# Optimization experiments

Hardware: AMD Instinct MI355X
Metric: run time of the kernel (lower is better)

## Reference

```python
import jax, jax.numpy as jnp
import numpy as np

D = 768      # embedding_dim
H = 12       # num_heads
HS = D // H  # head_size = 64
B, T, TC = 8, 1024, 256
FF = 4 * D
EPS = 1e-5


def _layernorm(x, w, b):
    mu = jnp.mean(x, axis=-1, keepdims=True)
    var = jnp.mean((x - mu) ** 2, axis=-1, keepdims=True)
    return (x - mu) / jnp.sqrt(var + EPS) * w + b


def _mha(x_q, x_kv, Wq, bq, Wk, bk, Wv, bv):
    # Batched equivalent of the per-head Python loop: weights stacked as [H, D, HS].
    q = jnp.einsum('btd,hde->bhte', x_q, Wq) + bq[None, :, None, :]
    k = jnp.einsum('bsd,hde->bhse', x_kv, Wk) + bk[None, :, None, :]
    v = jnp.einsum('bsd,hde->bhse', x_kv, Wv) + bv[None, :, None, :]
    scale = HS ** (-0.5)  # original scales by C**-0.5 with C = head_size
    wei = jax.nn.softmax(jnp.einsum('bhte,bhse->bhts', q, k) * scale, axis=-1)
    o = jnp.einsum('bhts,bhse->bhte', wei, v)  # [B,H,T,HS]
    # torch.cat over heads on dim=-1 == transpose then merge head dims
    return o.transpose(0, 2, 1, 3).reshape(o.shape[0], o.shape[2], H * HS)


def setup_inputs() -> dict:
    key = jax.random.key(0)
    ks = jax.random.split(key, 20)
    s = 0.02
    inp = {
        'img_embedding': jax.random.normal(ks[0], (B, T, D), jnp.float32),
        'context': jax.random.normal(ks[1], (B, TC, D), jnp.float32),
        'ln1_w': jnp.ones((D,), jnp.float32), 'ln1_b': jnp.zeros((D,), jnp.float32),
        'sWq': jax.random.normal(ks[2], (H, D, HS), jnp.float32) * s,
        'sbq': jnp.zeros((H, HS), jnp.float32),
        'sWk': jax.random.normal(ks[3], (H, D, HS), jnp.float32) * s,
        'sbk': jnp.zeros((H, HS), jnp.float32),
        'sWv': jax.random.normal(ks[4], (H, D, HS), jnp.float32) * s,
        'sbv': jnp.zeros((H, HS), jnp.float32),
        'ln2_w': jnp.ones((D,), jnp.float32), 'ln2_b': jnp.zeros((D,), jnp.float32),
        'cWq': jax.random.normal(ks[5], (H, D, HS), jnp.float32) * s,
        'cbq': jnp.zeros((H, HS), jnp.float32),
        'cWk': jax.random.normal(ks[6], (H, D, HS), jnp.float32) * s,
        'cbk': jnp.zeros((H, HS), jnp.float32),
        'cWv': jax.random.normal(ks[7], (H, D, HS), jnp.float32) * s,
        'cbv': jnp.zeros((H, HS), jnp.float32),
        'ln3_w': jnp.ones((D,), jnp.float32), 'ln3_b': jnp.zeros((D,), jnp.float32),
        'W1': jax.random.normal(ks[8], (D, FF), jnp.float32) * s,
        'b1': jnp.zeros((FF,), jnp.float32),
        'W2': jax.random.normal(ks[9], (FF, D), jnp.float32) * s,
        'b2': jnp.zeros((D,), jnp.float32),
    }
    return inp


def reference(img_embedding, context, ln1_w, ln1_b, sWq, sbq, sWk, sbk, sWv, sbv,
              ln2_w, ln2_b, cWq, cbq, cWk, cbk, cWv, cbv, ln3_w, ln3_b,
              W1, b1, W2, b2):
    x = img_embedding
    x = x + _mha(_layernorm(x, ln1_w, ln1_b), _layernorm(x, ln1_w, ln1_b),
                 sWq, sbq, sWk, sbk, sWv, sbv)
    x = x + _mha(_layernorm(x, ln2_w, ln2_b), context,
                 cWq, cbq, cWk, cbk, cWv, cbv)
    h = _layernorm(x, ln3_w, ln3_b)
    ff = jax.nn.silu(h @ W1 + b1) @ W2 + b2
    return x + ff
```

## Files before the change

kernel.cpp:

```cpp
#include <hip/hip_runtime.h>
#include <hip/hip_bf16.h>


#define D_EMB 768
#define N_HEADS 12
#define HEAD 64
#define B_SZ 8
#define T_IMG 1024
#define T_CTX 256
#define FF_DIM 3072
#define ROWS_IMG (B_SZ * T_IMG)
#define ROWS_CTX (B_SZ * T_CTX)
#define BIGCOL (1 << 28)
#define PART_STRIDE (ROWS_IMG * D_EMB)

typedef __bf16 bf16x8 __attribute__((ext_vector_type(8)));
typedef __bf16 bf16x4 __attribute__((ext_vector_type(4)));
typedef float f32x4 __attribute__((ext_vector_type(4)));

__device__ __forceinline__ void gld16(const void* g, void* l) {
    __builtin_amdgcn_global_load_lds(
        (const __attribute__((address_space(1))) unsigned int*)g,
        (__attribute__((address_space(3))) unsigned int*)l, 16, 0, 0);
}

__global__ __launch_bounds__(256) void reduce_w2_kernel(
    const __bf16* __restrict__ P, const float* __restrict__ b2,
    float* __restrict__ X) {
    int i = blockIdx.x * 256 + threadIdx.x;
    int base = i * 4;
    int col = base % D_EMB;
    bf16x4 p0 = *(const bf16x4*)&P[base];
    bf16x4 p1 = *(const bf16x4*)&P[PART_STRIDE + base];
    float4 x = *(float4*)&X[base];
    float4 bb = *(const float4*)&b2[col];
    x.x += (float)p0[0] + (float)p1[0] + bb.x;
    x.y += (float)p0[1] + (float)p1[1] + bb.y;
    x.z += (float)p0[2] + (float)p1[2] + bb.z;
    x.w += (float)p0[3] + (float)p1[3] + bb.w;
    *(float4*)&X[base] = x;
}

__device__ __forceinline__ void transpose_cvt_body(
    float (*tile)[65], const float* __restrict__ src, __bf16* __restrict__ dst,
    int src_rows, int src_cols, int bx, int by, int tid) {
    int r0 = by * 64, c0 = bx * 64;
    int lr = tid >> 4, lc = (tid & 15) * 4;
#pragma unroll
    for (int i = 0; i < 4; i++) {
        float4 v = *(const float4*)&src[(size_t)(r0 + i * 16 + lr) * src_cols + c0 + lc];
        tile[i * 16 + lr][lc] = v.x; tile[i * 16 + lr][lc + 1] = v.y;
        tile[i * 16 + lr][lc + 2] = v.z; tile[i * 16 + lr][lc + 3] = v.w;
    }
    __syncthreads();
#pragma unroll
    for (int i = 0; i < 4; i++) {
        int cc = i * 16 + lr;
        int rr = (tid & 15) * 4;
        bf16x4 o;
#pragma unroll
        for (int j = 0; j < 4; j++) o[j] = (__bf16)tile[rr + j][cc];
        *(bf16x4*)&dst[(size_t)(c0 + cc) * src_rows + r0 + rr] = o;
    }
}

__device__ __forceinline__ void repack_body(
    float (*tile)[65],
    const float* __restrict__ Wq, const float* __restrict__ Wk,
    const float* __restrict__ Wv, const float* __restrict__ bq,
    const float* __restrict__ bk, const float* __restrict__ bv,
    __bf16* __restrict__ Wt, float* __restrict__ bp, int bx, int byy, int tid) {
    int which = byy / 12, h = byy - which * 12;
    int d0 = bx * 64;
    const float* W = (which == 0) ? Wq : ((which == 1) ? Wk : Wv);
    const float* src = W + ((size_t)h * D_EMB + d0) * HEAD;
    int lr = tid >> 4, lc = (tid & 15) * 4;
#pragma unroll
    for (int i = 0; i < 4; i++) {
        float4 v = *(const float4*)&src[(size_t)(i * 16 + lr) * HEAD + lc];
        tile[i * 16 + lr][lc] = v.x; tile[i * 16 + lr][lc + 1] = v.y;
        tile[i * 16 + lr][lc + 2] = v.z; tile[i * 16 + lr][lc + 3] = v.w;
    }
    __syncthreads();
#pragma unroll
    for (int i = 0; i < 4; i++) {
        int e = i * 16 + lr;
        int dd = (tid & 15) * 4;
        bf16x4 o;
#pragma unroll
        for (int j = 0; j < 4; j++) o[j] = (__bf16)tile[dd + j][e];
        *(bf16x4*)&Wt[(size_t)(which * 768 + h * 64 + e) * D_EMB + d0 + dd] = o;
    }
    if (bx == 0 && tid < 64) {
        const float* bb = (which == 0) ? bq : ((which == 1) ? bk : bv);
        bp[which * 768 + h * 64 + tid] = bb[h * 64 + tid];
    }
}

__global__ __launch_bounds__(256) void preproc_kernel(
    const float* __restrict__ ctx, __bf16* __restrict__ ctxb,
    const float* __restrict__ sWq, const float* __restrict__ sWk,
    const float* __restrict__ sWv, const float* __restrict__ sbq,
    const float* __restrict__ sbk, const float* __restrict__ sbv,
    __bf16* __restrict__ Wt, float* __restrict__ bp,
    const float* __restrict__ cWq, const float* __restrict__ cWk,
    const float* __restrict__ cWv, const float* __restrict__ cbq,
    const float* __restrict__ cbk, const float* __restrict__ cbv,
    __bf16* __restrict__ cWt, float* __restrict__ cbp,
    const float* __restrict__ W1, __bf16* __restrict__ W1t,
    const float* __restrict__ W2, __bf16* __restrict__ W2t) {
    __shared__ float tile[64][65];
    int bid = blockIdx.x;
    int tid = threadIdx.x;
    if (bid < 1536) {
        int i = bid * 256 + tid;
        float4 v = ((const float4*)ctx)[i];
        __bf16* d = ctxb + i * 4;
        d[0] = (__bf16)v.x; d[1] = (__bf16)v.y; d[2] = (__bf16)v.z; d[3] = (__bf16)v.w;
    } else if (bid < 1968) {
        int vb = bid - 1536;
        repack_body(tile, sWq, sWk, sWv, sbq, sbk, sbv, Wt, bp,
                    vb % 12, vb / 12, tid);
    } else if (bid < 2400) {
        int vb = bid - 1968;
        repack_body(tile, cWq, cWk, cWv, cbq, cbk, cbv, cWt, cbp,
                    vb % 12, vb / 12, tid);
    } else if (bid < 2976) {
        int vb = bid - 2400;
        transpose_cvt_body(tile, W1, W1t, 768, FF_DIM, vb % 48, vb / 48, tid);
    } else {
        int vb = bid - 2976;
        transpose_cvt_body(tile, W2, W2t, FF_DIM, 768, vb % 12, vb / 12, tid);
    }
}

__global__ __launch_bounds__(256) void ln_kernel(const float* __restrict__ x,
                                                 const float* __restrict__ lw,
                                                 const float* __restrict__ lb,
                                                 __bf16* __restrict__ y) {
    int row = blockIdx.x;
    int tid = threadIdx.x;
    const float* xr = x + (size_t)row * D_EMB;
    float a0 = xr[tid], a1 = xr[tid + 256], a2 = xr[tid + 512];
    float s = a0 + a1 + a2;
    float ss = a0 * a0 + a1 * a1 + a2 * a2;
#pragma unroll
    for (int off = 32; off > 0; off >>= 1) {
        s += __shfl_down(s, off, 64);
        ss += __shfl_down(ss, off, 64);
    }
    __shared__ float red[8];
    __shared__ float stats[2];
    int wv = tid >> 6, lane = tid & 63;
    if (lane == 0) { red[wv] = s; red[4 + wv] = ss; }
    __syncthreads();
    if (tid == 0) {
        float S = red[0] + red[1] + red[2] + red[3];
        float SS = red[4] + red[5] + red[6] + red[7];
        float mu = S * (1.0f / D_EMB);
        float var = SS * (1.0f / D_EMB) - mu * mu;
        stats[0] = mu;
        stats[1] = rsqrtf(var + 1e-5f);
    }
    __syncthreads();
    float mu = stats[0], rs = stats[1];
    __bf16* yr = y + (size_t)row * D_EMB;
    yr[tid]       = (__bf16)((a0 - mu) * rs * lw[tid]       + lb[tid]);
    yr[tid + 256] = (__bf16)((a1 - mu) * rs * lw[tid + 256] + lb[tid + 256]);
    yr[tid + 512] = (__bf16)((a2 - mu) * rs * lw[tid + 512] + lb[tid + 512]);
}

__device__ __forceinline__ bf16x8 lds_frag(const __bf16* h, int row, int kk, int quad) {
    int off = (kk * 32 + quad * 8) ^ ((row & 7) << 3);
    return *(const bf16x8*)&h[row * 64 + off];
}

template <int LDA, int LDB>
__device__ __forceinline__ void gemm_body(
    int bx, int by, int kz, int tid,
    const __bf16* __restrict__ A,
    const __bf16* __restrict__ Bt,
    const float* __restrict__ bias,
    __bf16* __restrict__ Cb, int ldc,
    int Kc, int act, int qlimit,
    __bf16* __restrict__ VTout, int vtok, int vcol0, int kcol0, int kcol1,
    float* __restrict__ Xres,
    __bf16* As, __bf16* Bs) {
    int w = tid >> 6, lane = tid & 63;
    int c = lane & 15, quad = lane >> 4;
    int wm = (w >> 1) * 64, wn = (w & 1) * 64;

    f32x4 acc[4][4];
#pragma unroll
    for (int i = 0; i < 4; i++)
#pragma unroll
        for (int j = 0; j < 4; j++) acc[i][j] = (f32x4){0.f, 0.f, 0.f, 0.f};

    int srow = tid >> 3;
    int scol = ((tid & 7) * 8) ^ ((srow & 7) * 8);
    const __bf16* Ag = A + (size_t)(by * 128 + srow) * LDA + (size_t)kz * Kc + scol;
    const __bf16* Bg = Bt + (size_t)(bx * 128 + srow) * LDB + (size_t)kz * Kc + scol;
    char* AsB = (char*)As + w * 1024;
    char* BsB = (char*)Bs + w * 1024;

    for (int k0 = 0; k0 < Kc; k0 += 64) {
#pragma unroll
        for (int j = 0; j < 4; j++) {
            gld16(Ag + (size_t)(j * 32) * LDA + k0, AsB + j * 4096);
            gld16(Bg + (size_t)(j * 32) * LDB + k0, BsB + j * 4096);
        }
        __syncthreads();
#pragma unroll
        for (int kk = 0; kk < 2; kk++) {
            bf16x8 af[4], bfr[4];
#pragma unroll
            for (int mi = 0; mi < 4; mi++)
                af[mi] = lds_frag(As, wm + mi * 16 + c, kk, quad);
#pragma unroll
            for (int ni = 0; ni < 4; ni++)
                bfr[ni] = lds_frag(Bs, wn + ni * 16 + c, kk, quad);
#pragma unroll
            for (int mi = 0; mi < 4; mi++)
#pragma unroll
                for (int ni = 0; ni < 4; ni++)
                    acc[mi][ni] = __builtin_amdgcn_mfma_f32_16x16x32_bf16(
                        bfr[ni], af[mi], acc[mi][ni], 0, 0, 0);
        }
        __syncthreads();
    }

#pragma unroll
    for (int mi = 0; mi < 4; mi++) {
#pragma unroll
        for (int ni = 0; ni < 4; ni++) {
            int row = by * 128 + wm + mi * 16 + c;
            int colbase = bx * 128 + wn + ni * 16 + quad * 4;
            float bvv[4] = {0.f, 0.f, 0.f, 0.f};
            if (bias && kz == 0) {
                float4 b4 = *(const float4*)&bias[colbase];
                bvv[0] = b4.x; bvv[1] = b4.y; bvv[2] = b4.z; bvv[3] = b4.w;
            }
            float qs = (colbase < qlimit) ? 0.125f : 1.0f;
            float v[4];
#pragma unroll
            for (int r = 0; r < 4; r++) {
                float t = (acc[mi][ni][r] + bvv[r]) * qs;
                if (act == 1) t = t / (1.0f + __expf(-t));
                v[r] = t;
            }
            if (Xres) {
                float4 x4 = *(float4*)&Xres[(size_t)row * D_EMB + colbase];
                x4.x += v[0]; x4.y += v[1]; x4.z += v[2]; x4.w += v[3];
                *(float4*)&Xres[(size_t)row * D_EMB + colbase] = x4;
            } else if (VTout && colbase >= vcol0) {
                int hc = colbase - vcol0;
                int hh = hc >> 6, ebase = hc & 63;
                int tok = row;
#pragma unroll
                for (int r = 0; r < 4; r++) {
                    int e = ebase + r;
                    int sl = ((((tok >> 3) & 7) ^ (e & 7)) << 3) | (tok & 7);
                    VTout[(size_t)(hh * 64 + e) * vtok + (tok & ~63) + sl] = (__bf16)v[r];
                }
            } else if (colbase >= kcol0 && colbase < kcol1) {
                int hc = colbase - kcol0;
                int hh = hc >> 6, ebase = hc & 63;
                int tok = row;
                int es = (((ebase >> 3) ^ (tok & 7)) << 3) | (ebase & 7);
                bf16x4 pv;
#pragma unroll
                for (int r = 0; r < 4; r++) pv[r] = (__bf16)v[r];
                *(bf16x4*)&Cb[(size_t)tok * ldc + kcol0 + hh * 64 + es] = pv;
            } else {
                __bf16* dst = Cb + (size_t)kz * PART_STRIDE;
                bf16x4 pv;
#pragma unroll
                for (int r = 0; r < 4; r++) pv[r] = (__bf16)v[r];
                *(bf16x4*)&dst[(size_t)row * ldc + colbase] = pv;
            }
        }
    }
}

template <int LDA, int LDB>
__global__ __launch_bounds__(256) void mfma_gemm_bt(
    const __bf16* __restrict__ A,
    const __bf16* __restrict__ Bt,
    const float* __restrict__ bias,
    __bf16* __restrict__ Cb, int ldc,
    int Kc, int act, int qlimit,
    __bf16* __restrict__ VTout, int vtok, int vcol0, int kcol0, int kcol1,
    float* __restrict__ Xres) {
    __shared__ __bf16 As[128 * 64];
    __shared__ __bf16 Bs[128 * 64];
    int gx = gridDim.x;
    int nwg = gx * gridDim.y;
    int orig = blockIdx.y * gx + blockIdx.x;
    int swz = (orig & 7) * (nwg >> 3) + (orig >> 3);
    gemm_body<LDA, LDB>(swz % gx, swz / gx, blockIdx.z, threadIdx.x,
                        A, Bt, bias, Cb, ldc, Kc, act, qlimit,
                        VTout, vtok, vcol0, kcol0, kcol1, Xres, As, Bs);
}

__global__ __launch_bounds__(256) void cross_gemm_kernel(
    const __bf16* __restrict__ LNb, const __bf16* __restrict__ cWt,
    const float* __restrict__ cbp, const __bf16* __restrict__ ctxb,
    __bf16* __restrict__ Qc, __bf16* __restrict__ KVc,
    __bf16* __restrict__ VTc) {
    __shared__ __bf16 As[128 * 64];
    __shared__ __bf16 Bs[128 * 64];
    int bid = blockIdx.x;
    if (bid < 384) {
        int swz = (bid & 7) * 48 + (bid >> 3);
        gemm_body<768, 768>(swz % 6, swz / 6, 0, threadIdx.x,
                            LNb, cWt, cbp, Qc, 768, D_EMB, 0, 768,
                            nullptr, 0, BIGCOL, BIGCOL, BIGCOL, nullptr, As, Bs);
    } else {
        int b2 = bid - 384;
        int swz = (b2 & 7) * 24 + (b2 >> 3);
        gemm_body<768, 768>(swz % 12, swz / 12, 0, threadIdx.x,
                            ctxb, cWt + (size_t)768 * 768, cbp + 768,
                            KVc, 1536, D_EMB, 0, 0,
                            VTc, ROWS_CTX, 768, 0, 768, nullptr, As, Bs);
    }
}

__global__ __launch_bounds__(128, 2) void mfma_attn(
    const __bf16* __restrict__ Q, int qld,
    const __bf16* __restrict__ Kp, int kld,
    const __bf16* __restrict__ VTg, int vtok,
    int kv_tokens, float* __restrict__ X, const float* __restrict__ Xin) {
    __shared__ __bf16 Kt[64 * 64];
    __shared__ __bf16 VT[80 * 64];
    __shared__ __bf16 Ps[128 * 76];
    int tid = threadIdx.x;
    int bh = blockIdx.x % 96;
    int qt = blockIdx.x / 96;
    int b = bh / N_HEADS, h = bh - b * N_HEADS;
    int w = tid >> 6, lane = tid & 63, c = lane & 15, quad = lane >> 4;
    int q0 = qt * 128;

    for (int i = tid; i < 16 * 64; i += 128)
        VT[64 * 64 + i] = (i < 64) ? (__bf16)1.0f : (__bf16)0.0f;

    {
        const __bf16* Qg = Q + (size_t)(b * T_IMG + q0 + (tid >> 3)) * qld
                           + h * HEAD + (tid & 7) * 8;
        char* QsB = (char*)Ps + w * 1024;
#pragma unroll
        for (int j = 0; j < 8; j++)
            gld16(Qg + (size_t)j * 16 * qld, QsB + j * 2048);
    }
    __syncthreads();
    bf16x8 qa[4][2];
#pragma unroll
    for (int st = 0; st < 4; st++)
#pragma unroll
        for (int ch = 0; ch < 2; ch++)
            qa[st][ch] = *(const bf16x8*)&Ps[(w * 64 + st * 16 + c) * 64 + ch * 32 + quad * 8];
    __syncthreads();

    f32x4 o[4][5];
#pragma unroll
    for (int st = 0; st < 4; st++)
#pragma unroll
        for (int ut = 0; ut < 5; ut++) o[st][ut] = (f32x4){0.f, 0.f, 0.f, 0.f};

    char* KtB = (char*)Kt + w * 1024;
    char* VtB = (char*)VT + w * 1024;
    int ntiles = kv_tokens >> 6;
    for (int t = 0; t < ntiles; t++) {
        const __bf16* Kg = Kp + (size_t)(b * kv_tokens + t * 64 + (tid >> 3)) * kld
                           + h * HEAD + (tid & 7) * 8;
        const __bf16* Vg = VTg + (size_t)(h * HEAD + (tid >> 3)) * vtok
                           + b * kv_tokens + t * 64 + (tid & 7) * 8;
#pragma unroll
        for (int j = 0; j < 4; j++) {
            gld16(Kg + (size_t)j * 16 * kld, KtB + j * 2048);
            gld16(Vg + (size_t)j * 16 * vtok, VtB + j * 2048);
        }
        __syncthreads();

        bf16x8 kb[4][2];
#pragma unroll
        for (int nt = 0; nt < 4; nt++)
#pragma unroll
            for (int ch = 0; ch < 2; ch++)
                kb[nt][ch] = *(const bf16x8*)&Kt[(nt * 16 + c) * 64
                                + (((ch * 4 + quad) ^ (c & 7)) << 3)];
#pragma unroll
        for (int st = 0; st < 4; st++) {
            f32x4 s[4];
#pragma unroll
            for (int nt = 0; nt < 4; nt++) {
                s[nt] = (f32x4){0.f, 0.f, 0.f, 0.f};
                s[nt] = __builtin_amdgcn_mfma_f32_16x16x32_bf16(kb[nt][0], qa[st][0], s[nt], 0, 0, 0);
                s[nt] = __builtin_amdgcn_mfma_f32_16x16x32_bf16(kb[nt][1], qa[st][1], s[nt], 0, 0, 0);
            }
#pragma unroll
            for (int nt = 0; nt < 4; nt++) {
                bf16x4 pk;
#pragma unroll
                for (int r = 0; r < 4; r++) pk[r] = (__bf16)__expf(s[nt][r]);
                *(bf16x4*)&Ps[(size_t)(w * 64 + st * 16 + c) * 76 + nt * 16 + quad * 4] = pk;
            }
        }
        __syncthreads();

        bf16x8 vb[5][2];
#pragma unroll
        for (int ut = 0; ut < 5; ut++)
#pragma unroll
            for (int ch = 0; ch < 2; ch++)
                vb[ut][ch] = *(const bf16x8*)&VT[(ut * 16 + c) * 64
                                + (((ch * 4 + quad) ^ (c & 7)) << 3)];
#pragma unroll
        for (int st = 0; st < 4; st++) {
            bf16x8 pa0 = *(const bf16x8*)&Ps[(w * 64 + st * 16 + c) * 76 + quad * 8];
            bf16x8 pa1 = *(const bf16x8*)&Ps[(w * 64 + st * 16 + c) * 76 + 32 + quad * 8];
#pragma unroll
            for (int ut = 0; ut < 5; ut++) {
                o[st][ut] = __builtin_amdgcn_mfma_f32_16x16x32_bf16(pa0, vb[ut][0], o[st][ut], 0, 0, 0);
                o[st][ut] = __builtin_amdgcn_mfma_f32_16x16x32_bf16(pa1, vb[ut][1], o[st][ut], 0, 0, 0);
            }
        }
        __syncthreads();
    }

#pragma unroll
    for (int st = 0; st < 4; st++) {
        float lr[4];
#pragma unroll
        for (int r = 0; r < 4; r++) lr[r] = __shfl(o[st][4][r], lane & 48, 64);
#pragma unroll
        for (int ut = 0; ut < 4; ut++) {
#pragma unroll
            for (int r = 0; r < 4; r++) {
                int row = b * T_IMG + q0 + w * 64 + st * 16 + quad * 4 + r;
                int col = h * HEAD + ut * 16 + c;
                size_t idx = (size_t)row * D_EMB + col;
                float base = Xin ? Xin[idx] : X[idx];
                X[idx] = base + o[st][ut][r] / lr[r];
            }
        }
    }
}

extern "C" void kernel_launch(void* const* d_in, const int* in_sizes, int n_in,
                              void* d_out, int out_size, void* d_ws, size_t ws_size,
                              hipStream_t stream) {
    const float* img  = (const float*)d_in[0];
    const float* ctx  = (const float*)d_in[1];
    const float* ln1w = (const float*)d_in[2];  const float* ln1b = (const float*)d_in[3];
    const float* sWq  = (const float*)d_in[4];  const float* sbq  = (const float*)d_in[5];
    const float* sWk  = (const float*)d_in[6];  const float* sbk  = (const float*)d_in[7];
    const float* sWv  = (const float*)d_in[8];  const float* sbv  = (const float*)d_in[9];
    const float* ln2w = (const float*)d_in[10]; const float* ln2b = (const float*)d_in[11];
    const float* cWq  = (const float*)d_in[12]; const float* cbq  = (const float*)d_in[13];
    const float* cWk  = (const float*)d_in[14]; const float* cbk  = (const float*)d_in[15];
    const float* cWv  = (const float*)d_in[16]; const float* cbv  = (const float*)d_in[17];
    const float* ln3w = (const float*)d_in[18]; const float* ln3b = (const float*)d_in[19];
    const float* W1   = (const float*)d_in[20]; const float* b1   = (const float*)d_in[21];
    const float* W2   = (const float*)d_in[22]; const float* b2   = (const float*)d_in[23];

    float* X = (float*)d_out;

    char* p = (char*)d_ws;
    __bf16* LNb  = (__bf16*)p; p += (size_t)ROWS_IMG * D_EMB * 2;
    __bf16* VTg  = (__bf16*)p; p += (size_t)12 * 64 * ROWS_IMG * 2;
    __bf16* BIG  = (__bf16*)p; p += (size_t)ROWS_IMG * FF_DIM * 2;
    __bf16* ctxb = (__bf16*)p; p += (size_t)ROWS_CTX * D_EMB * 2;
    __bf16* Wt   = (__bf16*)p; p += (size_t)2304 * 768 * 2;
    __bf16* cWt  = (__bf16*)p; p += (size_t)2304 * 768 * 2;
    __bf16* W1t  = (__bf16*)p; p += (size_t)FF_DIM * 768 * 2;
    __bf16* W2t  = (__bf16*)p; p += (size_t)768 * FF_DIM * 2;
    __bf16* VTc  = (__bf16*)p; p += (size_t)12 * 64 * ROWS_CTX * 2;
    float*  bp   = (float*)p;  p += 2304 * 4;
    float*  cbp  = (float*)p;  p += 2304 * 4;
    __bf16* Pk   = LNb;
    __bf16* QKVb = BIG;
    __bf16* Qc   = BIG;
    __bf16* KVc  = BIG + (size_t)ROWS_IMG * 768;
    __bf16* FFh  = BIG;

    preproc_kernel<<<3552, 256, 0, stream>>>(
        ctx, ctxb,
        sWq, sWk, sWv, sbq, sbk, sbv, Wt, bp,
        cWq, cWk, cWv, cbq, cbk, cbv, cWt, cbp,
        W1, W1t, W2, W2t);

    ln_kernel<<<ROWS_IMG, 256, 0, stream>>>(img, ln1w, ln1b, LNb);
    mfma_gemm_bt<768, 768><<<dim3(2304 / 128, ROWS_IMG / 128), 256, 0, stream>>>(
        LNb, Wt, bp, QKVb, 2304, D_EMB, 0, 768,
        VTg, ROWS_IMG, 1536, 768, 1536, nullptr);
    mfma_attn<<<96 * 8, 128, 0, stream>>>(
        QKVb, 2304, QKVb + 768, 2304, VTg, ROWS_IMG, T_IMG, X, img);

    ln_kernel<<<ROWS_IMG, 256, 0, stream>>>(X, ln2w, ln2b, LNb);
    cross_gemm_kernel<<<576, 256, 0, stream>>>(LNb, cWt, cbp, ctxb, Qc, KVc, VTc);
    mfma_attn<<<96 * 8, 128, 0, stream>>>(
        Qc, 768, KVc, 1536, VTc, ROWS_CTX, T_CTX, X, nullptr);

    ln_kernel<<<ROWS_IMG, 256, 0, stream>>>(X, ln3w, ln3b, LNb);
    mfma_gemm_bt<768, 768><<<dim3(FF_DIM / 128, ROWS_IMG / 128), 256, 0, stream>>>(
        LNb, W1t, b1, FFh, FF_DIM, D_EMB, 1, 0,
        nullptr, 0, BIGCOL, BIGCOL, BIGCOL, nullptr);
    mfma_gemm_bt<3072, 3072><<<dim3(768 / 128, ROWS_IMG / 128, 2), 256, 0, stream>>>(
        FFh, W2t, nullptr, Pk, D_EMB, 1536, 0, 0,
        nullptr, 0, BIGCOL, BIGCOL, BIGCOL, nullptr);
    reduce_w2_kernel<<<ROWS_IMG * D_EMB / 4 / 256, 256, 0, stream>>>(Pk, b2, X);
}
```

Baseline: 475.5 us.

## Prefetch attention K/V tiles into registers and fuse first layernorm into preproc

The attention kernel now loads the next K/V tile from global memory into registers while the current tile is computed. Each tile is then written to shared memory after a barrier, replacing direct global-to-LDS loads issued at the start of each iteration. Two barriers per iteration are dropped, relying on each wave touching only its own rows of the P buffer. The first layernorm is folded into the preprocessing launch as extra blocks, saving one kernel launch. The cost is more registers in a kernel launched with occupancy 2, which could spill or lower occupancy.

After: 458.6 us. 3.6% less time.

```diff
diff --git a/kernel.cpp b/kernel.cpp
--- a/kernel.cpp
+++ b/kernel.cpp
@@ -97,6 +97,41 @@
     }
 }
 
+__device__ __forceinline__ void ln_body(const float* __restrict__ x,
+                                        const float* __restrict__ lw,
+                                        const float* __restrict__ lb,
+                                        __bf16* __restrict__ y,
+                                        int row, int tid) {
+    __shared__ float red[8];
+    __shared__ float stats[2];
+    const float* xr = x + (size_t)row * D_EMB;
+    float a0 = xr[tid], a1 = xr[tid + 256], a2 = xr[tid + 512];
+    float s = a0 + a1 + a2;
+    float ss = a0 * a0 + a1 * a1 + a2 * a2;
+#pragma unroll
+    for (int off = 32; off > 0; off >>= 1) {
+        s += __shfl_down(s, off, 64);
+        ss += __shfl_down(ss, off, 64);
+    }
+    int wv = tid >> 6, lane = tid & 63;
+    if (lane == 0) { red[wv] = s; red[4 + wv] = ss; }
+    __syncthreads();
+    if (tid == 0) {
+        float S = red[0] + red[1] + red[2] + red[3];
+        float SS = red[4] + red[5] + red[6] + red[7];
+        float mu = S * (1.0f / D_EMB);
+        float var = SS * (1.0f / D_EMB) - mu * mu;
+        stats[0] = mu;
+        stats[1] = rsqrtf(var + 1e-5f);
+    }
+    __syncthreads();
+    float mu = stats[0], rs = stats[1];
+    __bf16* yr = y + (size_t)row * D_EMB;
+    yr[tid]       = (__bf16)((a0 - mu) * rs * lw[tid]       + lb[tid]);
+    yr[tid + 256] = (__bf16)((a1 - mu) * rs * lw[tid + 256] + lb[tid + 256]);
+    yr[tid + 512] = (__bf16)((a2 - mu) * rs * lw[tid + 512] + lb[tid + 512]);
+}
+
 __global__ __launch_bounds__(256) void preproc_kernel(
     const float* __restrict__ ctx, __bf16* __restrict__ ctxb,
     const float* __restrict__ sWq, const float* __restrict__ sWk,
@@ -108,7 +143,9 @@
     const float* __restrict__ cbk, const float* __restrict__ cbv,
     __bf16* __restrict__ cWt, float* __restrict__ cbp,
     const float* __restrict__ W1, __bf16* __restrict__ W1t,
-    const float* __restrict__ W2, __bf16* __restrict__ W2t) {
+    const float* __restrict__ W2, __bf16* __restrict__ W2t,
+    const float* __restrict__ img, const float* __restrict__ ln1w,
+    const float* __restrict__ ln1b, __bf16* __restrict__ LNb) {
     __shared__ float tile[64][65];
     int bid = blockIdx.x;
     int tid = threadIdx.x;
@@ -128,9 +165,11 @@
     } else if (bid < 2976) {
         int vb = bid - 2400;
         transpose_cvt_body(tile, W1, W1t, 768, FF_DIM, vb % 48, vb / 48, tid);
-    } else {
+    } else if (bid < 3552) {
         int vb = bid - 2976;
         transpose_cvt_body(tile, W2, W2t, FF_DIM, 768, vb % 12, vb / 12, tid);
+    } else {
+        ln_body(img, ln1w, ln1b, LNb, bid - 3552, tid);
     }
 }
 
@@ -138,36 +177,7 @@
                                                  const float* __restrict__ lw,
                                                  const float* __restrict__ lb,
                                                  __bf16* __restrict__ y) {
-    int row = blockIdx.x;
-    int tid = threadIdx.x;
-    const float* xr = x + (size_t)row * D_EMB;
-    float a0 = xr[tid], a1 = xr[tid + 256], a2 = xr[tid + 512];
-    float s = a0 + a1 + a2;
-    float ss = a0 * a0 + a1 * a1 + a2 * a2;
-#pragma unroll
-    for (int off = 32; off > 0; off >>= 1) {
-        s += __shfl_down(s, off, 64);
-        ss += __shfl_down(ss, off, 64);
-    }
-    __shared__ float red[8];
-    __shared__ float stats[2];
-    int wv = tid >> 6, lane = tid & 63;
-    if (lane == 0) { red[wv] = s; red[4 + wv] = ss; }
-    __syncthreads();
-    if (tid == 0) {
-        float S = red[0] + red[1] + red[2] + red[3];
-        float SS = red[4] + red[5] + red[6] + red[7];
-        float mu = S * (1.0f / D_EMB);
-        float var = SS * (1.0f / D_EMB) - mu * mu;
-        stats[0] = mu;
-        stats[1] = rsqrtf(var + 1e-5f);
-    }
-    __syncthreads();
-    float mu = stats[0], rs = stats[1];
-    __bf16* yr = y + (size_t)row * D_EMB;
-    yr[tid]       = (__bf16)((a0 - mu) * rs * lw[tid]       + lb[tid]);
-    yr[tid + 256] = (__bf16)((a1 - mu) * rs * lw[tid + 256] + lb[tid + 256]);
-    yr[tid + 512] = (__bf16)((a2 - mu) * rs * lw[tid + 512] + lb[tid + 512]);
+    ln_body(x, lw, lb, y, blockIdx.x, threadIdx.x);
 }
 
 __device__ __forceinline__ bf16x8 lds_frag(const __bf16* h, int row, int kk, int quad) {
@@ -343,6 +353,17 @@
     for (int i = tid; i < 16 * 64; i += 128)
         VT[64 * 64 + i] = (i < 64) ? (__bf16)1.0f : (__bf16)0.0f;
 
+    const __bf16* Kg = Kp + (size_t)(b * kv_tokens + (tid >> 3)) * kld
+                       + h * HEAD + (tid & 7) * 8;
+    const __bf16* Vg = VTg + (size_t)(h * HEAD + (tid >> 3)) * vtok
+                       + b * kv_tokens + (tid & 7) * 8;
+    bf16x8 kr[4], vr[4], krn[4], vrn[4];
+#pragma unroll
+    for (int j = 0; j < 4; j++) {
+        kr[j] = *(const bf16x8*)(Kg + (size_t)(j * 16) * kld);
+        vr[j] = *(const bf16x8*)(Vg + (size_t)(j * 16) * vtok);
+    }
+
     {
         const __bf16* Qg = Q + (size_t)(b * T_IMG + q0 + (tid >> 3)) * qld
                            + h * HEAD + (tid & 7) * 8;
@@ -358,7 +379,6 @@
 #pragma unroll
         for (int ch = 0; ch < 2; ch++)
             qa[st][ch] = *(const bf16x8*)&Ps[(w * 64 + st * 16 + c) * 64 + ch * 32 + quad * 8];
-    __syncthreads();
 
     f32x4 o[4][5];
 #pragma unroll
@@ -366,20 +386,24 @@
 #pragma unroll
         for (int ut = 0; ut < 5; ut++) o[st][ut] = (f32x4){0.f, 0.f, 0.f, 0.f};
 
-    char* KtB = (char*)Kt + w * 1024;
-    char* VtB = (char*)VT + w * 1024;
     int ntiles = kv_tokens >> 6;
     for (int t = 0; t < ntiles; t++) {
-        const __bf16* Kg = Kp + (size_t)(b * kv_tokens + t * 64 + (tid >> 3)) * kld
-                           + h * HEAD + (tid & 7) * 8;
-        const __bf16* Vg = VTg + (size_t)(h * HEAD + (tid >> 3)) * vtok
-                           + b * kv_tokens + t * 64 + (tid & 7) * 8;
+        __syncthreads();
 #pragma unroll
         for (int j = 0; j < 4; j++) {
-            gld16(Kg + (size_t)j * 16 * kld, KtB + j * 2048);
-            gld16(Vg + (size_t)j * 16 * vtok, VtB + j * 2048);
+            *(bf16x8*)&Kt[tid * 8 + j * 1024] = kr[j];
+            *(bf16x8*)&VT[tid * 8 + j * 1024] = vr[j];
         }
         __syncthreads();
+        if (t + 1 < ntiles) {
+            const __bf16* Kg2 = Kg + (size_t)((t + 1) * 64) * kld;
+            const __bf16* Vg2 = Vg + (t + 1) * 64;
+#pragma unroll
+            for (int j = 0; j < 4; j++) {
+                krn[j] = *(const bf16x8*)(Kg2 + (size_t)(j * 16) * kld);
+                vrn[j] = *(const bf16x8*)(Vg2 + (size_t)(j * 16) * vtok);
+            }
+        }
 
         bf16x8 kb[4][2];
 #pragma unroll
@@ -405,7 +429,6 @@
                 *(bf16x4*)&Ps[(size_t)(w * 64 + st * 16 + c) * 76 + nt * 16 + quad * 4] = pk;
             }
         }
-        __syncthreads();
 
         bf16x8 vb[5][2];
 #pragma unroll
@@ -424,7 +447,10 @@
                 o[st][ut] = __builtin_amdgcn_mfma_f32_16x16x32_bf16(pa1, vb[ut][1], o[st][ut], 0, 0, 0);
             }
         }
-        __syncthreads();
+        if (t + 1 < ntiles) {
+#pragma unroll
+            for (int j = 0; j < 4; j++) { kr[j] = krn[j]; vr[j] = vrn[j]; }
+        }
     }
 
 #pragma unroll
@@ -483,13 +509,13 @@
     __bf16* KVc  = BIG + (size_t)ROWS_IMG * 768;
     __bf16* FFh  = BIG;
 
-    preproc_kernel<<<3552, 256, 0, stream>>>(
+    preproc_kernel<<<11744, 256, 0, stream>>>(
         ctx, ctxb,
         sWq, sWk, sWv, sbq, sbk, sbv, Wt, bp,
         cWq, cWk, cWv, cbq, cbk, cbv, cWt, cbp,
-        W1, W1t, W2, W2t);
-
-    ln_kernel<<<ROWS_IMG, 256, 0, stream>>>(img, ln1w, ln1b, LNb);
+        W1, W1t, W2, W2t,
+        img, ln1w, ln1b, LNb);
+
     mfma_gemm_bt<768, 768><<<dim3(2304 / 128, ROWS_IMG / 128), 256, 0, stream>>>(
         LNb, Wt, bp, QKVb, 2304, D_EMB, 0, 768,
         VTg, ROWS_IMG, 1536, 768, 1536, nullptr);
```
